# Kernel tuning notes

Measured on AMD Instinct MI355X. Metric: run time of the kernel, lower is better.

The kernel has to match this reference:

```python
import jax, jax.numpy as jnp
import numpy as np

B, N, I, O, R = 8, 1024, 256, 256, 8


def setup_inputs() -> dict:
    key = jax.random.key(0)
    k1, k2, k3 = jax.random.split(key, 3)
    x = jax.random.normal(k1, (B, N, I), dtype=jnp.float32)
    adj = jax.random.uniform(k2, (B, N, N, R), dtype=jnp.float32)  # soft adjacency [b, src, dst, r]
    weight = jax.random.normal(k3, (R, I, O), dtype=jnp.float32)   # per-relation transform
    return {"x": x, "adj": adj, "weight": weight}


def reference(x, adj, weight):
    # per-relation transformed features: [b, src, r, o]
    f = jnp.einsum('bni,rio->bnro', x, weight)
    # contraction over source nodes and relations, weighted by soft adjacency:
    # out[b, dst, o] = sum_{src, r} adj[b, src, dst, r] * f[b, src, r, o]
    out = jnp.einsum('bnro,bnmr->bmo', f, adj)
    # normalization: total incoming soft-edge weight per destination node
    denom = jnp.clip(adj.sum(axis=(1, 3)), 1e-16, None)  # [b, dst]
    return out / denom[..., None]
```

## Files before the change

kernel.cpp:

```cpp
#include <hip/hip_runtime.h>
#include <stdint.h>


typedef float          floatx4  __attribute__((ext_vector_type(4)));
typedef short          shortx8  __attribute__((ext_vector_type(8)));
typedef unsigned short ushortx4 __attribute__((ext_vector_type(4)));
typedef unsigned short ushortx8 __attribute__((ext_vector_type(8)));

__device__ __forceinline__ unsigned short f2bf(float f) {
  union { float f; unsigned int u; } v; v.f = f;
  unsigned int u = v.u + 0x7FFFu + ((v.u >> 16) & 1u);
  return (unsigned short)(u >> 16);
}

__device__ __forceinline__ void gload16(const void* g, void* l) {
  __builtin_amdgcn_global_load_lds((__attribute__((address_space(1))) void*)g,
                                   (__attribute__((address_space(3))) void*)l,
                                   16, 0, 0);
}

__global__ __launch_bounds__(256) void prep_x(const float* __restrict__ x,
                                              unsigned short* __restrict__ xbf) {
  int t = blockIdx.x * 256 + threadIdx.x;
  const float4* p = (const float4*)x + (size_t)t * 2;
  float4 a = p[0], b4 = p[1];
  ushortx8 o;
  o[0] = f2bf(a.x);  o[1] = f2bf(a.y);  o[2] = f2bf(a.z);  o[3] = f2bf(a.w);
  o[4] = f2bf(b4.x); o[5] = f2bf(b4.y); o[6] = f2bf(b4.z); o[7] = f2bf(b4.w);
  *(ushortx8*)(xbf + (size_t)t * 8) = o;
}

__global__ __launch_bounds__(256) void prep_w(const float* __restrict__ w,
                                              unsigned short* __restrict__ wt) {
  int id = blockIdx.x * 256 + threadIdx.x;
  int r = id >> 16, i = (id >> 8) & 255, o = id & 255;
  float v = w[((size_t)(r * 256 + i) << 8) + o];
  wt[((size_t)(o * 8 + r) << 8) + i] = f2bf(v);
}

__global__ __launch_bounds__(256) void k1_gemm(const unsigned short* __restrict__ xbf,
                                               const unsigned short* __restrict__ wt,
                                               unsigned short* __restrict__ ft) {
  int bid = blockIdx.x;
  int m0 = (bid >> 4) * 128, n0 = (bid & 15) * 128;
  int l = threadIdx.x & 63, w = threadIdx.x >> 6;
  int lr = l & 15, lg = l >> 4;
  int mw = m0 + (w >> 1) * 64, nw = n0 + (w & 1) * 64;

  floatx4 acc[4][4] = {};
#pragma unroll
  for (int ks = 0; ks < 8; ++ks) {
    shortx8 a[4], b[4];
#pragma unroll
    for (int mi = 0; mi < 4; ++mi)
      a[mi] = *(const shortx8*)(xbf + (size_t)(mw + mi * 16 + lr) * 256 + ks * 32 + lg * 8);
#pragma unroll
    for (int ni = 0; ni < 4; ++ni)
      b[ni] = *(const shortx8*)(wt + (size_t)(nw + ni * 16 + lr) * 256 + ks * 32 + lg * 8);
#pragma unroll
    for (int mi = 0; mi < 4; ++mi)
#pragma unroll
      for (int ni = 0; ni < 4; ++ni)
        acc[mi][ni] = __builtin_amdgcn_mfma_f32_16x16x32_bf16(a[mi], b[ni], acc[mi][ni], 0, 0, 0);
  }
#pragma unroll
  for (int mi = 0; mi < 4; ++mi) {
#pragma unroll
    for (int ni = 0; ni < 4; ++ni) {
      int np = nw + ni * 16 + lr;
      int o = np >> 3, r = np & 7;
#pragma unroll
      for (int reg = 0; reg < 4; ++reg) {
        int row = mw + mi * 16 + lg * 4 + reg;
        int b8 = row >> 10, src = row & 1023;
        ft[((size_t)(b8 * 256 + o) << 13) + src * 8 + r] = f2bf(acc[mi][ni][reg]);
      }
    }
  }
}

template <int KSPLIT>
__global__ __launch_bounds__(256) void k2_gemm(const float* __restrict__ adj,
                                               const unsigned short* __restrict__ ft,
                                               float* __restrict__ outp,
                                               float* __restrict__ pout,
                                               float* __restrict__ dpart) {
  __shared__ __align__(16) unsigned short Alds[32 * 64];
  __shared__ __align__(16) unsigned short Blds[256 * 64];
  __shared__ float dsums[256];
  __shared__ float denr[32];

  int bid = blockIdx.x;
  int kc = (KSPLIT == 2) ? (bid >> 8) : 0;
  int inner = bid & 255;
  int b = inner & 7;
  int dst0 = (inner >> 3) * 32;

  int t = threadIdx.x, l = t & 63, w = t >> 6;
  int lr = l & 15, lg = l >> 4;

  int dst_l = (t & 63) >> 1;
  int rh = (t & 1) * 4;
  int srcA = t >> 6;

  int orow_off = w * 8 + (l >> 3);
  int csw = (l & 7) ^ (l >> 3);

  const int KT = (KSPLIT == 2) ? 64 : 128;
  int src_base = kc * 512;
  const size_t adj_b = (size_t)b << 23;
  const unsigned short* ftb = ft + ((size_t)b << 21);

  float dsum = 0.f;
  floatx4 acc[2][4] = {};

  for (int kt = 0; kt < KT; ++kt) {
    int src0 = src_base + kt * 8;
    __syncthreads();
#pragma unroll
    for (int j = 0; j < 2; ++j) {
      int src_l = srcA + j * 4;
      const float* ap = adj + adj_b + (((size_t)(src0 + src_l) << 10) + dst0 + dst_l) * 8 + rh;
      float4 v = *(const float4*)ap;
      dsum += v.x + v.y + v.z + v.w;
      ushortx4 h;
      h[0] = f2bf(v.x); h[1] = f2bf(v.y); h[2] = f2bf(v.z); h[3] = f2bf(v.w);
      int slot = src_l ^ (dst_l & 7);
      *(ushortx4*)&Alds[dst_l * 64 + slot * 8 + rh] = h;
    }
    int kbase = src0 * 8;
#pragma unroll
    for (int i = 0; i < 8; ++i) {
      int orow = i * 32 + orow_off;
      const unsigned short* g = ftb + ((size_t)orow << 13) + kbase + (csw << 3);
      gload16(g, &Blds[(i * 32 + w * 8) * 64]);
    }
    __syncthreads();
#pragma unroll
    for (int s = 0; s < 2; ++s) {
      int slotbase = s * 4 + lg;
      shortx8 af[2], bfr[4];
#pragma unroll
      for (int mi = 0; mi < 2; ++mi) {
        int row = mi * 16 + lr;
        af[mi] = *(const shortx8*)&Alds[row * 64 + ((slotbase ^ (row & 7)) << 3)];
      }
#pragma unroll
      for (int ni = 0; ni < 4; ++ni) {
        int oc = w * 64 + ni * 16 + lr;
        bfr[ni] = *(const shortx8*)&Blds[oc * 64 + ((slotbase ^ (oc & 7)) << 3)];
      }
#pragma unroll
      for (int mi = 0; mi < 2; ++mi)
#pragma unroll
        for (int ni = 0; ni < 4; ++ni)
          acc[mi][ni] = __builtin_amdgcn_mfma_f32_16x16x32_bf16(af[mi], bfr[ni], acc[mi][ni], 0, 0, 0);
    }
  }

  dsums[t] = dsum;
  __syncthreads();
  if (t < 32) {
    float s = 0.f;
#pragma unroll
    for (int w2 = 0; w2 < 4; ++w2) {
      s += dsums[w2 * 64 + t * 2];
      s += dsums[w2 * 64 + t * 2 + 1];
    }
    denr[t] = s;
  }
  __syncthreads();

#pragma unroll
  for (int mi = 0; mi < 2; ++mi) {
#pragma unroll
    for (int reg = 0; reg < 4; ++reg) {
      int rl = mi * 16 + lg * 4 + reg;
      int row = dst0 + rl;
      float dinv = 0.f;
      if (KSPLIT == 1) dinv = 1.f / fmaxf(denr[rl], 1e-16f);
#pragma unroll
      for (int ni = 0; ni < 4; ++ni) {
        int col = w * 64 + ni * 16 + lr;
        float v = acc[mi][ni][reg];
        size_t idx = (((size_t)b << 10) + row) * 256 + col;
        if (KSPLIT == 1) outp[idx] = v * dinv;
        else             pout[(size_t)kc * 2097152 + idx] = v;
      }
    }
  }
  if (KSPLIT == 2 && t < 32) dpart[kc * 8192 + (b << 10) + dst0 + t] = denr[t];
}

__global__ __launch_bounds__(256) void k3_reduce(const float* __restrict__ pout,
                                                 const float* __restrict__ dpart,
                                                 float* __restrict__ outp) {
  int bid = blockIdx.x;
  size_t base = (size_t)bid * 256 + threadIdx.x;
  float v = pout[base] + pout[2097152 + base];
  float d = dpart[bid] + dpart[8192 + bid];
  outp[base] = v / fmaxf(d, 1e-16f);
}

extern "C" void kernel_launch(void* const* d_in, const int* in_sizes, int n_in,
                              void* d_out, int out_size, void* d_ws, size_t ws_size,
                              hipStream_t stream) {
  const float* x   = (const float*)d_in[0];
  const float* adj = (const float*)d_in[1];
  const float* w   = (const float*)d_in[2];
  float* out = (float*)d_out;

  char* ws = (char*)d_ws;
  unsigned short* ft  = (unsigned short*)(ws);
  unsigned short* xbf = (unsigned short*)(ws + 33554432);
  unsigned short* wt  = (unsigned short*)(ws + 37748736);
  float* pout  = (float*)(ws + 38797312);
  float* dpart = (float*)(ws + 55574528);

  prep_x<<<1024, 256, 0, stream>>>(x, xbf);
  prep_w<<<2048, 256, 0, stream>>>(w, wt);
  k1_gemm<<<1024, 256, 0, stream>>>(xbf, wt, ft);

  if (ws_size >= 55640064ull) {
    k2_gemm<2><<<512, 256, 0, stream>>>(adj, ft, out, pout, dpart);
    k3_reduce<<<8192, 256, 0, stream>>>(pout, dpart, out);
  } else {
    k2_gemm<1><<<256, 256, 0, stream>>>(adj, ft, out, pout, dpart);
  }
}
```

Before: 145.2 us.

## Double-buffer k2 LDS tiles with 512-thread blocks and merge prep kernels

Measured after the change: 149.8 us. 3.1% more time.

```diff
diff --git a/kernel.cpp b/kernel.cpp
--- a/kernel.cpp
+++ b/kernel.cpp
@@ -19,23 +19,25 @@
                                    16, 0, 0);
 }
 
-__global__ __launch_bounds__(256) void prep_x(const float* __restrict__ x,
-                                              unsigned short* __restrict__ xbf) {
-  int t = blockIdx.x * 256 + threadIdx.x;
-  const float4* p = (const float4*)x + (size_t)t * 2;
-  float4 a = p[0], b4 = p[1];
-  ushortx8 o;
-  o[0] = f2bf(a.x);  o[1] = f2bf(a.y);  o[2] = f2bf(a.z);  o[3] = f2bf(a.w);
-  o[4] = f2bf(b4.x); o[5] = f2bf(b4.y); o[6] = f2bf(b4.z); o[7] = f2bf(b4.w);
-  *(ushortx8*)(xbf + (size_t)t * 8) = o;
-}
-
-__global__ __launch_bounds__(256) void prep_w(const float* __restrict__ w,
-                                              unsigned short* __restrict__ wt) {
-  int id = blockIdx.x * 256 + threadIdx.x;
-  int r = id >> 16, i = (id >> 8) & 255, o = id & 255;
-  float v = w[((size_t)(r * 256 + i) << 8) + o];
-  wt[((size_t)(o * 8 + r) << 8) + i] = f2bf(v);
+__global__ __launch_bounds__(256) void prep_xw(const float* __restrict__ x,
+                                               const float* __restrict__ w,
+                                               unsigned short* __restrict__ xbf,
+                                               unsigned short* __restrict__ wt) {
+  int bid = blockIdx.x;
+  if (bid < 1024) {
+    int t = bid * 256 + threadIdx.x;
+    const float4* p = (const float4*)x + (size_t)t * 2;
+    float4 a = p[0], b4 = p[1];
+    ushortx8 o;
+    o[0] = f2bf(a.x);  o[1] = f2bf(a.y);  o[2] = f2bf(a.z);  o[3] = f2bf(a.w);
+    o[4] = f2bf(b4.x); o[5] = f2bf(b4.y); o[6] = f2bf(b4.z); o[7] = f2bf(b4.w);
+    *(ushortx8*)(xbf + (size_t)t * 8) = o;
+  } else {
+    int id = (bid - 1024) * 256 + threadIdx.x;
+    int r = id >> 16, i = (id >> 8) & 255, o = id & 255;
+    float v = w[((size_t)(r * 256 + i) << 8) + o];
+    wt[((size_t)(o * 8 + r) << 8) + i] = f2bf(v);
+  }
 }
 
 __global__ __launch_bounds__(256) void k1_gemm(const unsigned short* __restrict__ xbf,
@@ -79,76 +81,85 @@
   }
 }
 
-template <int KSPLIT>
-__global__ __launch_bounds__(256) void k2_gemm(const float* __restrict__ adj,
+#define BHALF 16384
+#define AHALF 4096
+__global__ __launch_bounds__(512) void k2_gemm(const float* __restrict__ adj,
                                                const unsigned short* __restrict__ ft,
-                                               float* __restrict__ outp,
                                                float* __restrict__ pout,
                                                float* __restrict__ dpart) {
-  __shared__ __align__(16) unsigned short Alds[32 * 64];
-  __shared__ __align__(16) unsigned short Blds[256 * 64];
-  __shared__ float dsums[256];
-  __shared__ float denr[32];
-
-  int bid = blockIdx.x;
-  int kc = (KSPLIT == 2) ? (bid >> 8) : 0;
-  int inner = bid & 255;
+  __shared__ __align__(16) unsigned short Blds[2 * BHALF];
+  __shared__ __align__(16) unsigned short Alds[2 * AHALF];
+  __shared__ float dsums[512];
+  __shared__ float denr[64];
+
+  int bid = blockIdx.x;
+  int kc = bid >> 7;
+  int inner = bid & 127;
   int b = inner & 7;
-  int dst0 = (inner >> 3) * 32;
+  int dst0 = (inner >> 3) * 64;
 
   int t = threadIdx.x, l = t & 63, w = t >> 6;
   int lr = l & 15, lg = l >> 4;
-
-  int dst_l = (t & 63) >> 1;
+  int wm = w >> 2, wo = w & 3;
+
+  int dst_l = (t >> 1) & 63;
   int rh = (t & 1) * 4;
-  int srcA = t >> 6;
-
-  int orow_off = w * 8 + (l >> 3);
+  int sA = t >> 7;
+
   int csw = (l & 7) ^ (l >> 3);
 
-  const int KT = (KSPLIT == 2) ? 64 : 128;
-  int src_base = kc * 512;
   const size_t adj_b = (size_t)b << 23;
   const unsigned short* ftb = ft + ((size_t)b << 21);
+  int src_base = kc * 512;
+  const int KT = 64;
 
   float dsum = 0.f;
   floatx4 acc[2][4] = {};
-
-  for (int kt = 0; kt < KT; ++kt) {
-    int src0 = src_base + kt * 8;
-    __syncthreads();
+  float4 av[2];
+
+  auto A_load = [&](int kt, float4* v) {
 #pragma unroll
     for (int j = 0; j < 2; ++j) {
-      int src_l = srcA + j * 4;
-      const float* ap = adj + adj_b + (((size_t)(src0 + src_l) << 10) + dst0 + dst_l) * 8 + rh;
-      float4 v = *(const float4*)ap;
-      dsum += v.x + v.y + v.z + v.w;
+      int src_l = sA + j * 4;
+      v[j] = *(const float4*)(adj + adj_b + ((size_t)(src_base + kt * 8 + src_l) << 13)
+                              + ((size_t)(dst0 + dst_l) << 3) + rh);
+    }
+  };
+  auto A_store = [&](int half, const float4* v) {
+#pragma unroll
+    for (int j = 0; j < 2; ++j) {
+      int src_l = sA + j * 4;
+      float4 q = v[j];
+      dsum += q.x + q.y + q.z + q.w;
       ushortx4 h;
-      h[0] = f2bf(v.x); h[1] = f2bf(v.y); h[2] = f2bf(v.z); h[3] = f2bf(v.w);
+      h[0] = f2bf(q.x); h[1] = f2bf(q.y); h[2] = f2bf(q.z); h[3] = f2bf(q.w);
       int slot = src_l ^ (dst_l & 7);
-      *(ushortx4*)&Alds[dst_l * 64 + slot * 8 + rh] = h;
-    }
-    int kbase = src0 * 8;
-#pragma unroll
-    for (int i = 0; i < 8; ++i) {
-      int orow = i * 32 + orow_off;
+      *(ushortx4*)&Alds[half * AHALF + dst_l * 64 + slot * 8 + rh] = h;
+    }
+  };
+  auto B_stage = [&](int kt, int half) {
+    int kbase = (src_base + kt * 8) * 8;
+#pragma unroll
+    for (int i = 0; i < 4; ++i) {
+      int orow = i * 64 + w * 8 + (l >> 3);
       const unsigned short* g = ftb + ((size_t)orow << 13) + kbase + (csw << 3);
-      gload16(g, &Blds[(i * 32 + w * 8) * 64]);
-    }
-    __syncthreads();
+      gload16(g, &Blds[half * BHALF + (i * 64 + w * 8) * 64]);
+    }
+  };
+  auto compute = [&](int half) {
 #pragma unroll
     for (int s = 0; s < 2; ++s) {
       int slotbase = s * 4 + lg;
       shortx8 af[2], bfr[4];
 #pragma unroll
       for (int mi = 0; mi < 2; ++mi) {
-        int row = mi * 16 + lr;
-        af[mi] = *(const shortx8*)&Alds[row * 64 + ((slotbase ^ (row & 7)) << 3)];
+        int row = wm * 32 + mi * 16 + lr;
+        af[mi] = *(const shortx8*)&Alds[half * AHALF + row * 64 + ((slotbase ^ (row & 7)) << 3)];
       }
 #pragma unroll
       for (int ni = 0; ni < 4; ++ni) {
-        int oc = w * 64 + ni * 16 + lr;
-        bfr[ni] = *(const shortx8*)&Blds[oc * 64 + ((slotbase ^ (oc & 7)) << 3)];
+        int oc = wo * 64 + ni * 16 + lr;
+        bfr[ni] = *(const shortx8*)&Blds[half * BHALF + oc * 64 + ((slotbase ^ (oc & 7)) << 3)];
       }
 #pragma unroll
       for (int mi = 0; mi < 2; ++mi)
@@ -156,16 +167,31 @@
         for (int ni = 0; ni < 4; ++ni)
           acc[mi][ni] = __builtin_amdgcn_mfma_f32_16x16x32_bf16(af[mi], bfr[ni], acc[mi][ni], 0, 0, 0);
     }
+  };
+
+  A_load(0, av);
+  B_stage(0, 0);
+  A_store(0, av);
+  __syncthreads();
+
+  for (int kt = 0; kt < KT; ++kt) {
+    int cur = kt & 1, nxt = cur ^ 1;
+    bool has = (kt + 1) < KT;
+    if (has) A_load(kt + 1, av);
+    if (has) B_stage(kt + 1, nxt);
+    compute(cur);
+    if (has) A_store(nxt, av);
+    __syncthreads();
   }
 
   dsums[t] = dsum;
   __syncthreads();
-  if (t < 32) {
+  if (t < 64) {
     float s = 0.f;
 #pragma unroll
-    for (int w2 = 0; w2 < 4; ++w2) {
-      s += dsums[w2 * 64 + t * 2];
-      s += dsums[w2 * 64 + t * 2 + 1];
+    for (int sh = 0; sh < 4; ++sh) {
+      s += dsums[sh * 128 + t * 2];
+      s += dsums[sh * 128 + t * 2 + 1];
     }
     denr[t] = s;
   }
@@ -175,21 +201,15 @@
   for (int mi = 0; mi < 2; ++mi) {
 #pragma unroll
     for (int reg = 0; reg < 4; ++reg) {
-      int rl = mi * 16 + lg * 4 + reg;
-      int row = dst0 + rl;
-      float dinv = 0.f;
-      if (KSPLIT == 1) dinv = 1.f / fmaxf(denr[rl], 1e-16f);
+      int row = dst0 + wm * 32 + mi * 16 + lg * 4 + reg;
 #pragma unroll
       for (int ni = 0; ni < 4; ++ni) {
-        int col = w * 64 + ni * 16 + lr;
-        float v = acc[mi][ni][reg];
-        size_t idx = (((size_t)b << 10) + row) * 256 + col;
-        if (KSPLIT == 1) outp[idx] = v * dinv;
-        else             pout[(size_t)kc * 2097152 + idx] = v;
-      }
-    }
-  }
-  if (KSPLIT == 2 && t < 32) dpart[kc * 8192 + (b << 10) + dst0 + t] = denr[t];
+        int col = wo * 64 + ni * 16 + lr;
+        pout[(size_t)kc * 2097152 + (((size_t)b << 10) + row) * 256 + col] = acc[mi][ni][reg];
+      }
+    }
+  }
+  if (t < 64) dpart[kc * 8192 + (b << 10) + dst0 + t] = denr[t];
 }
 
 __global__ __launch_bounds__(256) void k3_reduce(const float* __restrict__ pout,
@@ -217,14 +237,8 @@
   float* pout  = (float*)(ws + 38797312);
   float* dpart = (float*)(ws + 55574528);
 
-  prep_x<<<1024, 256, 0, stream>>>(x, xbf);
-  prep_w<<<2048, 256, 0, stream>>>(w, wt);
+  prep_xw<<<3072, 256, 0, stream>>>(x, w, xbf, wt);
   k1_gemm<<<1024, 256, 0, stream>>>(xbf, wt, ft);
-
-  if (ws_size >= 55640064ull) {
-    k2_gemm<2><<<512, 256, 0, stream>>>(adj, ft, out, pout, dpart);
-    k3_reduce<<<8192, 256, 0, stream>>>(pout, dpart, out);
-  } else {
-    k2_gemm<1><<<256, 256, 0, stream>>>(adj, ft, out, pout, dpart);
-  }
-}
+  k2_gemm<<<256, 512, 0, stream>>>(adj, ft, pout, dpart);
+  k3_reduce<<<8192, 256, 0, stream>>>(pout, dpart, out);
+}
```
